# Optimization experiments

Measured on AMD Instinct MI355X. Metric: run time of the kernel, lower is better.

## Reference

```python
import jax, jax.numpy as jnp
import numpy as np
import math

N, E, D, H, C, ED = 50000, 400000, 128, 8, 16, 64
HC = H * C  # == D (required by residual)
EPS = 1e-5


def _gelu(x):
    return 0.5 * x * (1.0 + jax.lax.erf(x / math.sqrt(2.0)))


def _layer_norm(x, g, b):
    m = jnp.mean(x, axis=-1, keepdims=True)
    v = jnp.mean(jnp.square(x - m), axis=-1, keepdims=True)
    return (x - m) * jax.lax.rsqrt(v + EPS) * g + b


def _batch_norm(x, g, b):
    # BatchNorm1d training-mode math: stats over the batch (row) dim
    m = jnp.mean(x, axis=0)
    v = jnp.mean(jnp.square(x - m), axis=0)
    return (x - m) * jax.lax.rsqrt(v + EPS) * g + b


def setup_inputs() -> dict:
    key = jax.random.key(0)
    ks = jax.random.split(key, 40)
    s = 0.05
    inp = {
        "x": jax.random.normal(ks[0], (N, D), jnp.float32),
        "edge_index": jax.random.randint(ks[1], (2, E), 0, N, jnp.int64),
        "edge_attr": jax.random.normal(ks[2], (E, ED), jnp.float32),
        # attention projections
        "Wq": jax.random.normal(ks[3], (D, HC), jnp.float32) * s,
        "bq": jnp.zeros((HC,), jnp.float32),
        "Wk": jax.random.normal(ks[4], (D, HC), jnp.float32) * s,
        "bk": jnp.zeros((HC,), jnp.float32),
        "Wv": jax.random.normal(ks[5], (D, HC), jnp.float32) * s,
        "bv": jnp.zeros((HC,), jnp.float32),
        "We": jax.random.normal(ks[6], (ED, HC), jnp.float32) * s,  # no bias
        "Wke": jax.random.normal(ks[7], (3 * C, C), jnp.float32) * s,
        "bke": jnp.zeros((C,), jnp.float32),
        "Wve": jax.random.normal(ks[8], (3 * C, C), jnp.float32) * s,
        "bve": jnp.zeros((C,), jnp.float32),
        "Wfce": jax.random.normal(ks[9], (HC, ED), jnp.float32) * s,
        "bfce": jnp.zeros((ED,), jnp.float32),
        "lne_g": jnp.ones((ED,), jnp.float32),
        "lne_b": jnp.zeros((ED,), jnp.float32),
        "Wfcn": jax.random.normal(ks[10], (HC, D), jnp.float32) * s,
        "bfcn": jnp.zeros((D,), jnp.float32),
        "lnn_g": jnp.ones((D,), jnp.float32),
        "lnn_b": jnp.zeros((D,), jnp.float32),
        # FFN
        "W1n": jax.random.normal(ks[11], (D, 4 * D), jnp.float32) * s,
        "b1n": jnp.zeros((4 * D,), jnp.float32),
        "W2n": jax.random.normal(ks[12], (4 * D, D), jnp.float32) * s,
        "b2n": jnp.zeros((D,), jnp.float32),
        "W1e": jax.random.normal(ks[13], (ED, 4 * ED), jnp.float32) * s,
        "b1e": jnp.zeros((4 * ED,), jnp.float32),
        "W2e": jax.random.normal(ks[14], (4 * ED, ED), jnp.float32) * s,
        "b2e": jnp.zeros((ED,), jnp.float32),
        "bnn_g": jnp.ones((D,), jnp.float32),
        "bnn_b": jnp.zeros((D,), jnp.float32),
        "bne_g": jnp.ones((ED,), jnp.float32),
        "bne_b": jnp.zeros((ED,), jnp.float32),
    }
    return inp


def _forward(x, edge_attr, Wq, bq, Wk, bk, Wv, bv, We, Wke, bke, Wve, bve,
             Wfce, bfce, lne_g, lne_b, Wfcn, bfcn, lnn_g, lnn_b,
             W1n, b1n, W2n, b2n, W1e, b1e, W2e, b2e,
             bnn_g, bnn_b, bne_g, bne_b, edge_index):
    src = edge_index[0]  # j (source)
    dst = edge_index[1]  # i (target / aggregation index)

    Q = (x @ Wq + bq).reshape(N, H, C)
    K = (x @ Wk + bk).reshape(N, H, C)
    V = (x @ Wv + bv).reshape(N, H, C)

    Qi = Q[dst]                                  # [E,H,C]
    e = (edge_attr @ We).reshape(E, H, C)        # W_e(edge_attr)

    # K_e(cat([K_i, K_j, e])) as three C x C matmuls (avoids big concat)
    Wk1, Wk2, Wk3 = Wke[:C], Wke[C:2 * C], Wke[2 * C:]
    Knew = (jnp.einsum('ehc,cd->ehd', K[dst], Wk1)
            + jnp.einsum('ehc,cd->ehd', K[src], Wk2)
            + jnp.einsum('ehc,cd->ehd', e, Wk3) + bke)

    logits = jnp.sum(Qi * Knew, axis=-1) / math.sqrt(C)   # [E,H]
    # segment softmax over target nodes (PyG softmax)
    mx = jax.ops.segment_max(logits, dst, num_segments=N)  # [N,H]
    ex = jnp.exp(logits - mx[dst])
    den = jax.ops.segment_sum(ex, dst, num_segments=N)
    alpha = ex / (den[dst] + 1e-16)                        # [E,H]

    Wv1, Wv2, Wv3 = Wve[:C], Wve[C:2 * C], Wve[2 * C:]
    Vnew = (jnp.einsum('ehc,cd->ehd', V[dst], Wv1)
            + jnp.einsum('ehc,cd->ehd', V[src], Wv2)
            + jnp.einsum('ehc,cd->ehd', e, Wv3) + bve)

    edge_store = e * alpha[..., None]                      # saved self.edge_attr
    msg = Vnew * alpha[..., None]
    out = jax.ops.segment_sum(msg, dst, num_segments=N)    # [N,H,C]

    e_out = _layer_norm(edge_store.reshape(E, HC) @ Wfce + bfce, lne_g, lne_b) + edge_attr
    x_out = _layer_norm(out.reshape(N, HC) @ Wfcn + bfcn, lnn_g, lnn_b) + x

    # PoswiseFeedForwardNetwork
    x2 = _batch_norm(_gelu(x_out @ W1n + b1n) @ W2n + b2n, bnn_g, bnn_b) + x_out
    e2 = _batch_norm(_gelu(e_out @ W1e + b1e) @ W2e + b2e, bne_g, bne_b) + e_out
    return jax.nn.softplus(x2), jax.nn.softplus(e2)


def reference(x, edge_index, edge_attr, Wq, bq, Wk, bk, Wv, bv, We, Wke, bke,
              Wve, bve, Wfce, bfce, lne_g, lne_b, Wfcn, bfcn, lnn_g, lnn_b,
              W1n, b1n, W2n, b2n, W1e, b1e, W2e, b2e, bnn_g, bnn_b, bne_g, bne_b):
    return _forward(x, edge_attr, Wq, bq, Wk, bk, Wv, bv, We, Wke, bke, Wve, bve,
                    Wfce, bfce, lne_g, lne_b, Wfcn, bfcn, lnn_g, lnn_b,
                    W1n, b1n, W2n, b2n, W1e, b1e, W2e, b2e,
                    bnn_g, bnn_b, bne_g, bne_b, edge_index)
```

## Files before the change

### kernel.cpp

```cpp
#include <hip/hip_runtime.h>
#include <math.h>
#include <stdint.h>

#define N_NODES 50000
#define E_EDGES 400000
#define DIM 128
#define HEADS 8
#define CH 16
#define EDIM 64
#define HCDIM 128

#define EPCHUNK 100000
#define NODE_WAVES 4

using bf16x8 = __attribute__((ext_vector_type(8))) short;
using f32x4v = __attribute__((ext_vector_type(4))) float;


__global__ void fill_kernel(float* p, float v, int n) {
    int i = blockIdx.x * blockDim.x + threadIdx.x;
    if (i < n) p[i] = v;
}

__global__ void concat3_kernel(const float* __restrict__ a, const float* __restrict__ b,
                               const float* __restrict__ c, float* __restrict__ o) {
    int i = blockIdx.x * 256 + threadIdx.x;
    if (i < 128) o[i] = a[i];
    else if (i < 256) o[i] = b[i - 128];
    else if (i < 384) o[i] = c[i - 256];
}

__device__ inline float gelu_f(float x) {
    return 0.5f * x * (1.0f + erff(x * 0.70710678118654752f));
}

__device__ inline float softplus_f(float x) {
    return x > 20.f ? x : log1pf(expf(x));
}

__device__ inline unsigned short f32_to_bf16_rn(float f) {
    unsigned u = __float_as_uint(f);
    u += 0x7FFFu + ((u >> 16) & 1u);
    return (unsigned short)(u >> 16);
}
__device__ inline float bf16_to_f32(unsigned short h) {
    return __uint_as_float((unsigned)h << 16);
}

__global__ __launch_bounds__(256) void wsplit_kernel(
    const float* __restrict__ W, unsigned short* __restrict__ hi,
    unsigned short* __restrict__ lo, int K, int N)
{
    int idx = blockIdx.x * 256 + threadIdx.x;
    if (idx >= K * N) return;
    int n = idx / K, k = idx - n * K;
    float x = W[(size_t)k * N + n];
    unsigned short h = f32_to_bf16_rn(x);
    hi[idx] = h;
    lo[idx] = f32_to_bf16_rn(x - bf16_to_f32(h));
}

__global__ __launch_bounds__(256) void wsplit_perm_kernel(
    const float* __restrict__ W, unsigned short* __restrict__ hi,
    unsigned short* __restrict__ lo, int K, int N)
{
    int idx = blockIdx.x * 256 + threadIdx.x;
    if (idx >= K * N) return;
    int n = idx / K, k = idx - n * K;
    int s = k & 31, base = k & ~31;
    int lgp = s >> 3, j = s & 7;
    int ksrc = base + ((j < 4) ? (lgp * 4 + j) : (16 + lgp * 4 + (j - 4)));
    float x = W[(size_t)ksrc * N + n];
    unsigned short h = f32_to_bf16_rn(x);
    hi[idx] = h;
    lo[idx] = f32_to_bf16_rn(x - bf16_to_f32(h));
}

template<int BN>
__global__ __launch_bounds__(256) void gemm_mfma(
    const float* __restrict__ A,
    const unsigned short* __restrict__ Whi, const unsigned short* __restrict__ Wlo,
    const float* __restrict__ bias, const float* __restrict__ ascale,
    float* __restrict__ C, int M, int K, int Nc, int act, int cmode)
{
    constexpr int MT = (BN == 128) ? 4 : 2;
    __shared__ bf16x8 As[2][4][128];

    const int tid = threadIdx.x;
    const int w = tid >> 6, lane = tid & 63;
    const int l15 = lane & 15, lg = lane >> 4;
    const int m0 = blockIdx.y * 128;
    const int n0 = blockIdx.x * BN;
    const int rowbase = (BN == 128) ? (w >> 1) * 64 : w * 32;
    const int colbase = (BN == 128) ? (w & 1) * 64 : 0;
    const int k16 = K >> 4;

    f32x4v acc[MT][4];
#pragma unroll
    for (int i = 0; i < MT; ++i)
#pragma unroll
        for (int j = 0; j < 4; ++j)
#pragma unroll
            for (int cidx = 0; cidx < 4; ++cidx) acc[i][j][cidx] = 0.f;

    for (int k0 = 0; k0 < K; k0 += 32) {
#pragma unroll
        for (int it = 0; it < 2; ++it) {
            int row = w * 16 + l15 + it * 64;
            int ar = m0 + row;
            float v[8];
            if (ar < M) {
                const float* ap = A + (size_t)ar * K + k0 + lg * 8;
                *(float4*)&v[0] = *(const float4*)ap;
                *(float4*)&v[4] = *(const float4*)(ap + 4);
                if (ascale) {
                    float s = ascale[(size_t)ar * k16 + ((k0 >> 4) + (lg >> 1))];
#pragma unroll
                    for (int j = 0; j < 8; ++j) v[j] *= s;
                }
            } else {
#pragma unroll
                for (int j = 0; j < 8; ++j) v[j] = 0.f;
            }
            bf16x8 gh, gl;
#pragma unroll
            for (int j = 0; j < 8; ++j) {
                unsigned short h = f32_to_bf16_rn(v[j]);
                gh[j] = (short)h;
                gl[j] = (short)f32_to_bf16_rn(v[j] - bf16_to_f32(h));
            }
            As[0][lg][row] = gh;
            As[1][lg][row] = gl;
        }
        bf16x8 bh[4], bl[4];
#pragma unroll
        for (int nt = 0; nt < 4; ++nt) {
            size_t off = (size_t)(n0 + colbase + nt * 16 + l15) * K + k0 + lg * 8;
            bh[nt] = *(const bf16x8*)(Whi + off);
            bl[nt] = *(const bf16x8*)(Wlo + off);
        }
        __syncthreads();
#pragma unroll
        for (int mt = 0; mt < MT; ++mt) {
            int arow = rowbase + mt * 16 + l15;
            bf16x8 ah = As[0][lg][arow];
            bf16x8 al = As[1][lg][arow];
#pragma unroll
            for (int nt = 0; nt < 4; ++nt) {
                acc[mt][nt] = __builtin_amdgcn_mfma_f32_16x16x32_bf16(ah, bh[nt], acc[mt][nt], 0, 0, 0);
                acc[mt][nt] = __builtin_amdgcn_mfma_f32_16x16x32_bf16(al, bh[nt], acc[mt][nt], 0, 0, 0);
                acc[mt][nt] = __builtin_amdgcn_mfma_f32_16x16x32_bf16(ah, bl[nt], acc[mt][nt], 0, 0, 0);
            }
        }
        __syncthreads();
    }

#pragma unroll
    for (int nt = 0; nt < 4; ++nt) {
        int col = n0 + colbase + nt * 16 + l15;
        float bb = bias ? bias[col] : 0.f;
#pragma unroll
        for (int mt = 0; mt < MT; ++mt) {
#pragma unroll
            for (int i = 0; i < 4; ++i) {
                int r = m0 + rowbase + mt * 16 + lg * 4 + i;
                if (r < M) {
                    float o = acc[mt][nt][i] + bb;
                    if (act == 1) o = gelu_f(o);
                    if (cmode == 1) {
                        C[(size_t)(col >> 7) * ((size_t)N_NODES * HCDIM) + (size_t)r * HCDIM + (col & 127)] = o;
                    } else {
                        C[(size_t)r * Nc + col] = o;
                    }
                }
            }
        }
    }
}

static inline void launch_mfma(const float* A, const unsigned short* Whi, const unsigned short* Wlo,
                               const float* bias, const float* ascale, float* C,
                               int M, int K, int Nc, int act, int cmode, hipStream_t stream)
{
    int gy = (M + 127) / 128;
    if (Nc % 128 == 0)
        gemm_mfma<128><<<dim3(Nc / 128, gy), dim3(256), 0, stream>>>(A, Whi, Wlo, bias, ascale, C, M, K, Nc, act, cmode);
    else
        gemm_mfma<64><<<dim3(Nc / 64, gy), dim3(256), 0, stream>>>(A, Whi, Wlo, bias, ascale, C, M, K, Nc, act, cmode);
}

template<int MT, int K1, int NH, int N2, int ACT1, int ASC, int LN2>
__global__ __launch_bounds__(256) void ffn2_nobar(
    const float* __restrict__ A,
    const unsigned short* __restrict__ W1hi, const unsigned short* __restrict__ W1lo,
    const float* __restrict__ b1,
    const unsigned short* __restrict__ W2hi, const unsigned short* __restrict__ W2lo,
    const float* __restrict__ b2,
    const float* __restrict__ ascale,
    const float* __restrict__ lng, const float* __restrict__ lnb,
    const float* __restrict__ resid,
    float* __restrict__ Cout, int M)
{
    constexpr int NK = K1 / 32;
    constexpr int NT2 = N2 / 16;
    constexpr int NI = NH / 16;
    constexpr int NP = NH / 32;
    const int tid = threadIdx.x;
    const int w = tid >> 6, lane = tid & 63;
    const int l15 = lane & 15, lg = lane >> 4;
    const int row0 = (blockIdx.x * 4 + w) * (MT * 16);

    bf16x8 aAh[MT][NK], aAl[MT][NK];
#pragma unroll
    for (int mt = 0; mt < MT; ++mt) {
        int r = row0 + mt * 16 + l15;
#pragma unroll
        for (int ks = 0; ks < NK; ++ks) {
            float v[8];
            if (r < M) {
                const float* ap = A + (size_t)r * K1 + ks * 32 + lg * 8;
                *(float4*)&v[0] = *(const float4*)ap;
                *(float4*)&v[4] = *(const float4*)(ap + 4);
            } else {
#pragma unroll
                for (int j = 0; j < 8; ++j) v[j] = 0.f;
            }
            bf16x8 gh, gl;
#pragma unroll
            for (int j = 0; j < 8; ++j) {
                unsigned short h = f32_to_bf16_rn(v[j]);
                gh[j] = (short)h;
                gl[j] = (short)f32_to_bf16_rn(v[j] - bf16_to_f32(h));
            }
            aAh[mt][ks] = gh;
            aAl[mt][ks] = gl;
        }
    }

    f32x4v oacc[MT][NT2];
#pragma unroll
    for (int mt = 0; mt < MT; ++mt)
#pragma unroll
        for (int nt = 0; nt < NT2; ++nt)
#pragma unroll
            for (int c = 0; c < 4; ++c) oacc[mt][nt][c] = 0.f;

    for (int p = 0; p < NP; ++p) {
        bf16x8 hh[MT], hl[MT];
#pragma unroll
        for (int half = 0; half < 2; ++half) {
            const int it = p * 2 + half;
            f32x4v h[MT];
#pragma unroll
            for (int mt = 0; mt < MT; ++mt)
#pragma unroll
                for (int c = 0; c < 4; ++c) h[mt][c] = 0.f;
#pragma unroll
            for (int ks = 0; ks < NK; ++ks) {
                size_t off = (size_t)(it * 16 + l15) * K1 + ks * 32 + lg * 8;
                bf16x8 xh = *(const bf16x8*)(W1hi + off);
                bf16x8 xl = *(const bf16x8*)(W1lo + off);
#pragma unroll
                for (int mt = 0; mt < MT; ++mt) {
                    h[mt] = __builtin_amdgcn_mfma_f32_16x16x32_bf16(xh, aAh[mt][ks], h[mt], 0, 0, 0);
                    h[mt] = __builtin_amdgcn_mfma_f32_16x16x32_bf16(xl, aAh[mt][ks], h[mt], 0, 0, 0);
                    h[mt] = __builtin_amdgcn_mfma_f32_16x16x32_bf16(xh, aAl[mt][ks], h[mt], 0, 0, 0);
                }
            }
            float b1a[4] = {0.f, 0.f, 0.f, 0.f};
            if (b1) *(float4*)b1a = *(const float4*)(b1 + it * 16 + lg * 4);
#pragma unroll
            for (int mt = 0; mt < MT; ++mt) {
                float sc = 1.f;
                if (ASC) {
                    int r = row0 + mt * 16 + l15;
                    sc = (r < M) ? ascale[(size_t)r * NI + it] : 0.f;
                }
#pragma unroll
                for (int i = 0; i < 4; ++i) {
                    float o = h[mt][i] + b1a[i];
                    if (ACT1) o = gelu_f(o);
                    if (ASC) o *= sc;
                    unsigned short oh = f32_to_bf16_rn(o);
                    hh[mt][half * 4 + i] = (short)oh;
                    hl[mt][half * 4 + i] = (short)f32_to_bf16_rn(o - bf16_to_f32(oh));
                }
            }
        }
#pragma unroll
        for (int nt2 = 0; nt2 < NT2; ++nt2) {
            size_t off2 = (size_t)(nt2 * 16 + l15) * NH + p * 32 + lg * 8;
            bf16x8 x2h = *(const bf16x8*)(W2hi + off2);
            bf16x8 x2l = *(const bf16x8*)(W2lo + off2);
#pragma unroll
            for (int mt = 0; mt < MT; ++mt) {
                oacc[mt][nt2] = __builtin_amdgcn_mfma_f32_16x16x32_bf16(x2h, hh[mt], oacc[mt][nt2], 0, 0, 0);
                oacc[mt][nt2] = __builtin_amdgcn_mfma_f32_16x16x32_bf16(x2l, hh[mt], oacc[mt][nt2], 0, 0, 0);
                oacc[mt][nt2] = __builtin_amdgcn_mfma_f32_16x16x32_bf16(x2h, hl[mt], oacc[mt][nt2], 0, 0, 0);
            }
        }
    }

    float b2a[NT2][4];
#pragma unroll
    for (int nt2 = 0; nt2 < NT2; ++nt2) {
        if (b2) *(float4*)b2a[nt2] = *(const float4*)(b2 + nt2 * 16 + lg * 4);
        else { b2a[nt2][0] = 0.f; b2a[nt2][1] = 0.f; b2a[nt2][2] = 0.f; b2a[nt2][3] = 0.f; }
    }
    if (LN2) {
        float ga[NT2][4], bba[NT2][4];
#pragma unroll
        for (int nt2 = 0; nt2 < NT2; ++nt2) {
            *(float4*)ga[nt2] = *(const float4*)(lng + nt2 * 16 + lg * 4);
            *(float4*)bba[nt2] = *(const float4*)(lnb + nt2 * 16 + lg * 4);
        }
#pragma unroll
        for (int mt = 0; mt < MT; ++mt) {
            int r = row0 + mt * 16 + l15;
            float o[NT2][4];
            float s = 0.f;
#pragma unroll
            for (int nt2 = 0; nt2 < NT2; ++nt2)
#pragma unroll
                for (int i = 0; i < 4; ++i) { o[nt2][i] = oacc[mt][nt2][i] + b2a[nt2][i]; s += o[nt2][i]; }
            s += __shfl_xor(s, 16); s += __shfl_xor(s, 32);
            float mean = s * (1.f / (float)N2);
            float q = 0.f;
#pragma unroll
            for (int nt2 = 0; nt2 < NT2; ++nt2)
#pragma unroll
                for (int i = 0; i < 4; ++i) { o[nt2][i] -= mean; q += o[nt2][i] * o[nt2][i]; }
            q += __shfl_xor(q, 16); q += __shfl_xor(q, 32);
            float inv = rsqrtf(q * (1.f / (float)N2) + 1e-5f);
            if (r < M) {
#pragma unroll
                for (int nt2 = 0; nt2 < NT2; ++nt2) {
                    float4 rv = *(const float4*)(resid + (size_t)r * N2 + nt2 * 16 + lg * 4);
                    float4 ov;
                    ov.x = o[nt2][0] * inv * ga[nt2][0] + bba[nt2][0] + rv.x;
                    ov.y = o[nt2][1] * inv * ga[nt2][1] + bba[nt2][1] + rv.y;
                    ov.z = o[nt2][2] * inv * ga[nt2][2] + bba[nt2][2] + rv.z;
                    ov.w = o[nt2][3] * inv * ga[nt2][3] + bba[nt2][3] + rv.w;
                    *(float4*)(Cout + (size_t)r * N2 + nt2 * 16 + lg * 4) = ov;
                }
            }
        }
    } else {
#pragma unroll
        for (int mt = 0; mt < MT; ++mt) {
            int r = row0 + mt * 16 + l15;
            if (r < M) {
#pragma unroll
                for (int nt2 = 0; nt2 < NT2; ++nt2) {
                    float4 ov;
                    ov.x = oacc[mt][nt2][0] + b2a[nt2][0];
                    ov.y = oacc[mt][nt2][1] + b2a[nt2][1];
                    ov.z = oacc[mt][nt2][2] + b2a[nt2][2];
                    ov.w = oacc[mt][nt2][3] + b2a[nt2][3];
                    *(float4*)(Cout + (size_t)r * N2 + nt2 * 16 + lg * 4) = ov;
                }
            }
        }
    }
}

__global__ __launch_bounds__(256) void wex_kernel(
    const float* __restrict__ We, const float* __restrict__ X, float* __restrict__ out)
{
    int idx = blockIdx.x * 256 + threadIdx.x;
    if (idx >= 64 * 128) return;
    int k = idx >> 7, hj = idx & 127, h = hj >> 4, j = hj & 15;
    float s = 0.f;
#pragma unroll
    for (int c = 0; c < 16; ++c) s += We[k * 128 + h * 16 + c] * X[c * 16 + j];
    out[idx] = s;
}

__global__ __launch_bounds__(256) void qk_pre_kernel(
    const float* __restrict__ Q, const float* __restrict__ K,
    const float* __restrict__ Wke, const float* __restrict__ bke,
    float* __restrict__ A2, float* __restrict__ c0)
{
    __shared__ float wk1[256], wk2[256], bks[16];
    for (int i = threadIdx.x; i < 256; i += 256) { wk1[i] = Wke[i]; wk2[i] = Wke[256 + i]; }
    if (threadIdx.x < 16) bks[threadIdx.x] = bke[threadIdx.x];
    __syncthreads();
    int idx = blockIdx.x * 256 + threadIdx.x;
    int j = idx & 15; int dh = idx >> 4; int h = dh & 7; int d = dh >> 3;
    if (d >= N_NODES) return;
    const float* q = Q + (size_t)d * HCDIM + h * CH;
    const float* k = K + (size_t)d * HCDIM + h * CH;
    float qv[16], kv[16];
#pragma unroll
    for (int t = 0; t < 4; ++t) {
        *(float4*)&qv[t * 4] = *(const float4*)(q + t * 4);
        *(float4*)&kv[t * 4] = *(const float4*)(k + t * 4);
    }
    float a2 = 0.f;
#pragma unroll
    for (int t = 0; t < 16; ++t) a2 += wk2[j * 16 + t] * qv[t];
    A2[idx] = a2;
    float kn = bks[j];
#pragma unroll
    for (int c = 0; c < 16; ++c) kn += kv[c] * wk1[c * 16 + j];
    float t = qv[j] * kn;
    t += __shfl_xor(t, 1); t += __shfl_xor(t, 2); t += __shfl_xor(t, 4); t += __shfl_xor(t, 8);
    if (j == 0) c0[dh] = t;
}

__global__ __launch_bounds__(256) void logits_kernel(
    const float* __restrict__ Q, const float* __restrict__ K,
    const float* __restrict__ A2, const float* __restrict__ c0,
    const float* __restrict__ ep3,
    const int* __restrict__ src, const int* __restrict__ dst,
    float* __restrict__ logits, int e0, int ecnt)
{
    int idx = blockIdx.x * 256 + threadIdx.x;
    if (idx >= ecnt * HEADS) return;
    int el = idx >> 3, h = idx & 7, e = e0 + el;
    int s = src[e], d = dst[e];
    const float* q  = Q  + (size_t)d * HCDIM + h * CH;
    const float* a2 = A2 + (size_t)d * HCDIM + h * CH;
    const float* ks = K  + (size_t)s * HCDIM + h * CH;
    const float* ep = ep3 + (size_t)el * HCDIM + h * CH;
    float acc = c0[(size_t)d * HEADS + h];
    float qv[16], av[16], kv[16], ev[16];
#pragma unroll
    for (int t = 0; t < 4; ++t) {
        *(float4*)&qv[t * 4] = *(const float4*)(q + t * 4);
        *(float4*)&av[t * 4] = *(const float4*)(a2 + t * 4);
        *(float4*)&kv[t * 4] = *(const float4*)(ks + t * 4);
        *(float4*)&ev[t * 4] = *(const float4*)(ep + t * 4);
    }
#pragma unroll
    for (int t = 0; t < 16; ++t) acc += av[t] * kv[t] + qv[t] * ev[t];
    logits[(size_t)e * HEADS + h] = acc * 0.25f;
}

__global__ __launch_bounds__(256) void count_kernel(const int* __restrict__ dst, int* __restrict__ cnt) {
    int e = blockIdx.x * 256 + threadIdx.x;
    if (e < E_EDGES) atomicAdd(&cnt[dst[e]], 1);
}

__global__ __launch_bounds__(1024) void scan_kernel(
    const int* __restrict__ cnt, int* __restrict__ rowptr, int* __restrict__ cursor, int n)
{
    __shared__ int buf[1024];
    __shared__ int base;
    int tid = threadIdx.x;
    if (tid == 0) { base = 0; rowptr[0] = 0; }
    __syncthreads();
    for (int t0 = 0; t0 < n; t0 += 1024) {
        int i = t0 + tid;
        int v = (i < n) ? cnt[i] : 0;
        buf[tid] = v;
        __syncthreads();
        for (int off = 1; off < 1024; off <<= 1) {
            int add = (tid >= off) ? buf[tid - off] : 0;
            __syncthreads();
            buf[tid] += add;
            __syncthreads();
        }
        if (i < n) { rowptr[i + 1] = base + buf[tid]; cursor[i] = base + buf[tid] - v; }
        __syncthreads();
        if (tid == 0) base += buf[1023];
        __syncthreads();
    }
}

__global__ __launch_bounds__(256) void scatter_kernel(
    const int* __restrict__ dst, int* __restrict__ cursor, int* __restrict__ eidx) {
    int e = blockIdx.x * 256 + threadIdx.x;
    if (e < E_EDGES) {
        int p = atomicAdd(&cursor[dst[e]], 1);
        eidx[p] = e;
    }
}

__global__ __launch_bounds__(256) void node_attn_kernel(
    const float* __restrict__ Vb, const float* __restrict__ edge_attr,
    float* __restrict__ logits,
    const int* __restrict__ rowptr, const int* __restrict__ eidx,
    const int* __restrict__ src,
    const float* __restrict__ Wve, const float* __restrict__ bve,
    const float* __restrict__ WeWv3, float* __restrict__ aggout)
{
    __shared__ float wv1s[256], wv2s[256], bvs[16];
    __shared__ float stage[NODE_WAVES][640];

    for (int i = threadIdx.x; i < 256; i += 256) { wv1s[i] = Wve[i]; wv2s[i] = Wve[256 + i]; }
    if (threadIdx.x < 16) bvs[threadIdx.x] = bve[threadIdx.x];
    __syncthreads();

    int w = threadIdx.x >> 6, lane = threadIdx.x & 63;
    int d = blockIdx.x * NODE_WAVES + w;
    int r0 = rowptr[d], r1 = rowptr[d + 1], deg = r1 - r0;
    int h = lane >> 3, kg = lane & 7;

    if (deg == 0) {
        aggout[(size_t)d * HCDIM + lane] = 0.f;
        aggout[(size_t)d * HCDIM + 64 + lane] = 0.f;
    } else {
        float m[8], ssum[8];
#pragma unroll
        for (int t = 0; t < 8; ++t) { m[t] = -INFINITY; ssum[t] = 0.f; }
        for (int i = r0 + lane; i < r1; i += 64) {
            int e = eidx[i];
            const float* lp = logits + (size_t)e * HEADS;
            float l[8];
            *(float4*)&l[0] = *(const float4*)lp;
            *(float4*)&l[4] = *(const float4*)(lp + 4);
#pragma unroll
            for (int t = 0; t < 8; ++t) m[t] = fmaxf(m[t], l[t]);
        }
#pragma unroll
        for (int o = 1; o < 64; o <<= 1) {
#pragma unroll
            for (int t = 0; t < 8; ++t) m[t] = fmaxf(m[t], __shfl_xor(m[t], o));
        }
        for (int i = r0 + lane; i < r1; i += 64) {
            int e = eidx[i];
            const float* lp = logits + (size_t)e * HEADS;
            float l[8];
            *(float4*)&l[0] = *(const float4*)lp;
            *(float4*)&l[4] = *(const float4*)(lp + 4);
#pragma unroll
            for (int t = 0; t < 8; ++t) ssum[t] += expf(l[t] - m[t]);
        }
#pragma unroll
        for (int o = 1; o < 64; o <<= 1) {
#pragma unroll
            for (int t = 0; t < 8; ++t) ssum[t] += __shfl_xor(ssum[t], o);
        }
        float mh = m[0], dd = ssum[0];
#pragma unroll
        for (int t = 1; t < 8; ++t) { if (h == t) { mh = m[t]; dd = ssum[t]; } }
        float den = dd + 1e-16f;

        float wea[8] = {0.f, 0.f, 0.f, 0.f, 0.f, 0.f, 0.f, 0.f};
        float av0 = 0.f, av1 = 0.f;
        for (int i = r0; i < r1; ++i) {
            int e = eidx[i];
            float lg = logits[(size_t)e * HEADS + h];
            float alpha = expf(lg - mh) / den;
            if (kg == 0) logits[(size_t)e * HEADS + h] = alpha;
            int s = src[e];
            const float* ea = edge_attr + (size_t)e * EDIM + kg * 8;
            float ev[8];
            *(float4*)&ev[0] = *(const float4*)ea;
            *(float4*)&ev[4] = *(const float4*)(ea + 4);
#pragma unroll
            for (int t = 0; t < 8; ++t) wea[t] += alpha * ev[t];
            float2 vv = *(const float2*)(Vb + (size_t)s * HCDIM + h * CH + kg * 2);
            av0 += alpha * vv.x;
            av1 += alpha * vv.y;
        }
        float* st = stage[w];
#pragma unroll
        for (int t = 0; t < 8; ++t) st[h * 64 + kg * 8 + t] = wea[t];
        st[512 + h * 16 + kg * 2] = av0;
        st[512 + h * 16 + kg * 2 + 1] = av1;
    }
    __syncthreads();
    if (deg > 0) {
        float* st = stage[w];
        int c0i = kg * 2;
        float acc0 = bvs[c0i], acc1 = bvs[c0i + 1];
        const float* vd = Vb + (size_t)d * HCDIM + h * CH;
#pragma unroll
        for (int j = 0; j < 16; ++j) {
            float vj = vd[j];
            float a = st[512 + h * 16 + j];
            acc0 += vj * wv1s[j * 16 + c0i] + a * wv2s[j * 16 + c0i];
            acc1 += vj * wv1s[j * 16 + c0i + 1] + a * wv2s[j * 16 + c0i + 1];
        }
        const float* w3 = WeWv3 + h * 16 + c0i;
#pragma unroll 16
        for (int k = 0; k < 64; ++k) {
            float wv = st[h * 64 + k];
            float2 w2v = *(const float2*)(w3 + k * 128);
            acc0 += wv * w2v.x;
            acc1 += wv * w2v.y;
        }
        aggout[(size_t)d * HCDIM + h * CH + c0i] = acc0;
        aggout[(size_t)d * HCDIM + h * CH + c0i + 1] = acc1;
    }
}

__global__ __launch_bounds__(256) void ln_res_kernel(
    float* __restrict__ y, const float* __restrict__ g, const float* __restrict__ b,
    const float* __restrict__ res, int rows, int w)
{
    int wave = threadIdx.x >> 6;
    int lane = threadIdx.x & 63;
    int nw = blockDim.x >> 6;
    for (int r = blockIdx.x * nw + wave; r < rows; r += gridDim.x * nw) {
        size_t base = (size_t)r * w;
        float v0 = y[base + lane];
        float v1 = (w == 128) ? y[base + 64 + lane] : 0.f;
        float s = v0 + v1;
#pragma unroll
        for (int o = 32; o; o >>= 1) s += __shfl_xor(s, o);
        float m = s / (float)w;
        float d0 = v0 - m;
        float d1 = (w == 128) ? (v1 - m) : 0.f;
        float q = d0 * d0 + d1 * d1;
#pragma unroll
        for (int o = 32; o; o >>= 1) q += __shfl_xor(q, o);
        float inv = rsqrtf(q / (float)w + 1e-5f);
        y[base + lane] = d0 * inv * g[lane] + b[lane] + res[base + lane];
        if (w == 128)
            y[base + 64 + lane] = d1 * inv * g[64 + lane] + b[64 + lane] + res[base + 64 + lane];
    }
}

__global__ __launch_bounds__(256) void bn_stats_kernel(
    const float* __restrict__ y, float* __restrict__ colsum, float* __restrict__ colsq,
    int rows, int cols)
{
    __shared__ float ss[256], sq[256];
    int tid = threadIdx.x;
    int col = tid % cols;
    int rsub = tid / cols;
    int rstep = blockDim.x / cols;
    float ls = 0.f, lq = 0.f;
    for (int r = blockIdx.x * rstep + rsub; r < rows; r += gridDim.x * rstep) {
        float v = y[(size_t)r * cols + col];
        ls += v;
        lq += v * v;
    }
    ss[tid] = ls;
    sq[tid] = lq;
    __syncthreads();
    if (tid < cols) {
        for (int o = cols; o < 256; o += cols) { ls += ss[tid + o]; lq += sq[tid + o]; }
        atomicAdd(&colsum[tid], ls);
        atomicAdd(&colsq[tid], lq);
    }
}

__global__ __launch_bounds__(256) void bn_apply_softplus_kernel(
    const float* __restrict__ y, const float* __restrict__ res,
    const float* __restrict__ colsum, const float* __restrict__ colsq,
    const float* __restrict__ g, const float* __restrict__ b,
    float* __restrict__ out, int rows, int cols)
{
    int idx = blockIdx.x * blockDim.x + threadIdx.x;
    int n = rows * cols;
    if (idx >= n) return;
    int c = idx % cols;
    float m = colsum[c] / (float)rows;
    float var = colsq[c] / (float)rows - m * m;
    float inv = rsqrtf(var + 1e-5f);
    float v = (y[idx] - m) * inv * g[c] + b[c] + res[idx];
    out[idx] = softplus_f(v);
}


extern "C" void kernel_launch(void* const* d_in, const int* in_sizes, int n_in,
                              void* d_out, int out_size, void* d_ws, size_t ws_size,
                              hipStream_t stream) {
    const float* x         = (const float*)d_in[0];
    const int*   ei        = (const int*)d_in[1];
    const float* edge_attr = (const float*)d_in[2];
    const float* Wq  = (const float*)d_in[3];
    const float* bq  = (const float*)d_in[4];
    const float* Wk  = (const float*)d_in[5];
    const float* bk  = (const float*)d_in[6];
    const float* Wv  = (const float*)d_in[7];
    const float* bv  = (const float*)d_in[8];
    const float* We  = (const float*)d_in[9];
    const float* Wke = (const float*)d_in[10];
    const float* bke = (const float*)d_in[11];
    const float* Wve = (const float*)d_in[12];
    const float* bve = (const float*)d_in[13];
    const float* Wfce = (const float*)d_in[14];
    const float* bfce = (const float*)d_in[15];
    const float* lne_g = (const float*)d_in[16];
    const float* lne_b = (const float*)d_in[17];
    const float* Wfcn = (const float*)d_in[18];
    const float* bfcn = (const float*)d_in[19];
    const float* lnn_g = (const float*)d_in[20];
    const float* lnn_b = (const float*)d_in[21];
    const float* W1n = (const float*)d_in[22];
    const float* b1n = (const float*)d_in[23];
    const float* W2n = (const float*)d_in[24];
    const float* b2n = (const float*)d_in[25];
    const float* W1e = (const float*)d_in[26];
    const float* b1e = (const float*)d_in[27];
    const float* W2e = (const float*)d_in[28];
    const float* b2e = (const float*)d_in[29];
    const float* bnn_g = (const float*)d_in[30];
    const float* bnn_b = (const float*)d_in[31];
    const float* bne_g = (const float*)d_in[32];
    const float* bne_b = (const float*)d_in[33];

    const int* src = ei;
    const int* dst = ei + E_EDGES;

    float* ws = (float*)d_ws;
    const size_t M64   = (size_t)E_EDGES * EDIM;
    const size_t NODE2 = (size_t)N_NODES * HCDIM;

    float* regionR = ws;
    float* Qb  = regionR;
    float* Kb  = regionR + NODE2;
    float* Vb  = regionR + 2 * NODE2;

    float* overlayY = ws + M64;
    float* logits = overlayY;
    float* c0buf  = logits + (size_t)E_EDGES * HEADS;
    int*   cnt_i    = (int*)(c0buf + (size_t)N_NODES * HEADS);
    int*   rowptr_i = cnt_i + N_NODES;
    int*   cursor_i = rowptr_i + N_NODES + 1;
    int*   eidx_i   = cursor_i + N_NODES;
    float* aggout = (float*)(((uintptr_t)(eidx_i + E_EDGES) + 15) & ~(uintptr_t)15);
    float* y_n    = aggout + NODE2;
    float* x_out  = y_n + NODE2;
    float* y_e    = overlayY;
    float* epbig  = y_n;

    float* e_out = ws + 2 * M64;
    float* A2buf = e_out;

    float* tail = ws + 3 * M64;
    float* colsum_n = tail;
    float* colsq_n  = tail + 128;
    float* colsum_e = tail + 256;
    float* colsq_e  = tail + 320;
    float* WeK3  = tail + 384;
    float* WeWv3 = WeK3 + 8192;
    float* bqkv  = WeWv3 + 8192;

    unsigned short* wsp = (unsigned short*)(bqkv + 384);
    unsigned short* QKV_s  = wsp;
    unsigned short* WeK3_s = QKV_s  + 2 * 49152;
    unsigned short* We_s   = WeK3_s + 2 * 8192;
    unsigned short* Wfce_s = We_s   + 2 * 8192;
    unsigned short* Wfcn_s = Wfce_s + 2 * 8192;
    unsigned short* W1n_s  = Wfcn_s + 2 * 16384;
    unsigned short* W2n_s  = W1n_s  + 2 * 65536;
    unsigned short* W1e_s  = W2n_s  + 2 * 65536;
    unsigned short* W2e_s  = W1e_s  + 2 * 16384;

    dim3 blk(256);

    fill_kernel<<<dim3(2), blk, 0, stream>>>(colsum_n, 0.f, 384);
    fill_kernel<<<dim3((N_NODES + 255) / 256), blk, 0, stream>>>((float*)cnt_i, 0.f, N_NODES);

    wex_kernel<<<dim3(32), blk, 0, stream>>>(We, Wke + 2 * CH * CH, WeK3);
    wex_kernel<<<dim3(32), blk, 0, stream>>>(We, Wve + 2 * CH * CH, WeWv3);

    wsplit_kernel<<<dim3(64), blk, 0, stream>>>(Wq, QKV_s,          QKV_s + 49152,          128, 128);
    wsplit_kernel<<<dim3(64), blk, 0, stream>>>(Wk, QKV_s + 16384,  QKV_s + 49152 + 16384,  128, 128);
    wsplit_kernel<<<dim3(64), blk, 0, stream>>>(Wv, QKV_s + 32768,  QKV_s + 49152 + 32768,  128, 128);
    wsplit_kernel<<<dim3(32), blk, 0, stream>>>(WeK3, WeK3_s, WeK3_s + 8192,  64, 128);
    wsplit_kernel<<<dim3(32), blk, 0, stream>>>(We,   We_s,   We_s + 8192,    64, 128);
    wsplit_perm_kernel<<<dim3(32), blk, 0, stream>>>(Wfce, Wfce_s, Wfce_s + 8192,  128, 64);
    wsplit_kernel<<<dim3(64), blk, 0, stream>>>(Wfcn, Wfcn_s, Wfcn_s + 16384, 128, 128);
    wsplit_kernel<<<dim3(256), blk, 0, stream>>>(W1n, W1n_s, W1n_s + 65536,   128, 512);
    wsplit_perm_kernel<<<dim3(256), blk, 0, stream>>>(W2n, W2n_s, W2n_s + 65536,   512, 128);
    wsplit_kernel<<<dim3(64), blk, 0, stream>>>(W1e, W1e_s, W1e_s + 16384,    64, 256);
    wsplit_perm_kernel<<<dim3(64), blk, 0, stream>>>(W2e, W2e_s, W2e_s + 16384,    256, 64);
    concat3_kernel<<<dim3(2), blk, 0, stream>>>(bq, bk, bv, bqkv);

    launch_mfma(x, QKV_s, QKV_s + 49152, bqkv, nullptr, Qb, N_NODES, 128, 384, 0, 1, stream);

    qk_pre_kernel<<<dim3(N_NODES * HCDIM / 256), blk, 0, stream>>>(Qb, Kb, Wke, bke, A2buf, c0buf);

    count_kernel<<<dim3((E_EDGES + 255) / 256), blk, 0, stream>>>(dst, cnt_i);
    scan_kernel<<<dim3(1), dim3(1024), 0, stream>>>(cnt_i, rowptr_i, cursor_i, N_NODES);
    scatter_kernel<<<dim3((E_EDGES + 255) / 256), blk, 0, stream>>>(dst, cursor_i, eidx_i);

    for (int e0 = 0; e0 < E_EDGES; e0 += EPCHUNK) {
        launch_mfma(edge_attr + (size_t)e0 * EDIM, WeK3_s, WeK3_s + 8192, nullptr, nullptr,
                    epbig, EPCHUNK, EDIM, HCDIM, 0, 0, stream);
        logits_kernel<<<dim3((EPCHUNK * HEADS + 255) / 256), blk, 0, stream>>>(
            Qb, Kb, A2buf, c0buf, epbig, src, dst, logits, e0, EPCHUNK);
    }

    node_attn_kernel<<<dim3(N_NODES / NODE_WAVES), blk, 0, stream>>>(
        Vb, edge_attr, logits, rowptr_i, eidx_i, src, Wve, bve, WeWv3, aggout);

    ffn2_nobar<2, 64, 128, 64, 0, 1, 1><<<dim3(E_EDGES / 128), blk, 0, stream>>>(
        edge_attr, We_s, We_s + 8192, nullptr, Wfce_s, Wfce_s + 8192, bfce,
        logits, lne_g, lne_b, edge_attr, e_out, E_EDGES);

    launch_mfma(aggout, Wfcn_s, Wfcn_s + 16384, bfcn, nullptr, x_out, N_NODES, HCDIM, DIM, 0, 0, stream);
    ln_res_kernel<<<dim3(12500), blk, 0, stream>>>(x_out, lnn_g, lnn_b, x, N_NODES, DIM);

    ffn2_nobar<1, 128, 512, 128, 1, 0, 0><<<dim3((N_NODES + 63) / 64), blk, 0, stream>>>(
        x_out, W1n_s, W1n_s + 65536, b1n, W2n_s, W2n_s + 65536, b2n,
        nullptr, nullptr, nullptr, nullptr, y_n, N_NODES);
    bn_stats_kernel<<<dim3(256), blk, 0, stream>>>(y_n, colsum_n, colsq_n, N_NODES, DIM);
    {
        int n = N_NODES * DIM;
        bn_apply_softplus_kernel<<<dim3((n + 255) / 256), blk, 0, stream>>>(
            y_n, x_out, colsum_n, colsq_n, bnn_g, bnn_b, (float*)d_out, N_NODES, DIM);
    }

    ffn2_nobar<2, 64, 256, 64, 1, 0, 0><<<dim3(E_EDGES / 128), blk, 0, stream>>>(
        e_out, W1e_s, W1e_s + 16384, b1e, W2e_s, W2e_s + 16384, b2e,
        nullptr, nullptr, nullptr, nullptr, y_e, E_EDGES);
    bn_stats_kernel<<<dim3(256), blk, 0, stream>>>(y_e, colsum_e, colsq_e, E_EDGES, EDIM);
    {
        int n = E_EDGES * EDIM;
        bn_apply_softplus_kernel<<<dim3((n + 255) / 256), blk, 0, stream>>>(
            y_e, e_out, colsum_e, colsq_e, bne_g, bne_b, (float*)d_out + (size_t)N_NODES * DIM, E_EDGES, EDIM);
    }
}
```

Measured before the change: 2.043 ms.

## Fuse edge projection GEMM with logits computation and streamline softmax

Replaces the chunked edge-projection GEMM plus separate logits kernel with a single MFMA kernel that computes the per-edge projection in registers and reduces it directly into attention logits. This avoids writing and re-reading a 400000x128 float intermediate and drops eight launches. It also adds a single-pass softmax path for nodes with at most 64 incoming edges and pads the shared staging buffer to reduce LDS bank conflicts. In exchange, the fused epilogue does uncoalesced scalar gathers of Q/A2/K rows per lane and uses shuffle reductions.

```diff
diff --git a/kernel.cpp b/kernel.cpp
--- a/kernel.cpp
+++ b/kernel.cpp
@@ -10,7 +10,6 @@
 #define EDIM 64
 #define HCDIM 128
 
-#define EPCHUNK 100000
 #define NODE_WAVES 4
 
 using bf16x8 = __attribute__((ext_vector_type(8))) short;
@@ -189,6 +188,102 @@
         gemm_mfma<64><<<dim3(Nc / 64, gy), dim3(256), 0, stream>>>(A, Whi, Wlo, bias, ascale, C, M, K, Nc, act, cmode);
 }
 
+__global__ __launch_bounds__(256) void eproj_logits_kernel(
+    const float* __restrict__ EA,
+    const unsigned short* __restrict__ Whi, const unsigned short* __restrict__ Wlo,
+    const float* __restrict__ Qp, const float* __restrict__ Kp,
+    const float* __restrict__ A2, const float* __restrict__ c0,
+    const int* __restrict__ src, const int* __restrict__ dst,
+    float* __restrict__ logits)
+{
+    __shared__ bf16x8 As[2][4][128];
+    const int tid = threadIdx.x;
+    const int w = tid >> 6, lane = tid & 63;
+    const int l15 = lane & 15, lg = lane >> 4;
+    const int m0 = blockIdx.x * 128;
+    const int rowbase = (w >> 1) * 64;
+    const int colbase = (w & 1) * 64;
+
+    f32x4v acc[4][4];
+#pragma unroll
+    for (int i = 0; i < 4; ++i)
+#pragma unroll
+        for (int j = 0; j < 4; ++j)
+#pragma unroll
+            for (int cidx = 0; cidx < 4; ++cidx) acc[i][j][cidx] = 0.f;
+
+    for (int k0 = 0; k0 < EDIM; k0 += 32) {
+#pragma unroll
+        for (int it = 0; it < 2; ++it) {
+            int row = w * 16 + l15 + it * 64;
+            const float* ap = EA + (size_t)(m0 + row) * EDIM + k0 + lg * 8;
+            float v[8];
+            *(float4*)&v[0] = *(const float4*)ap;
+            *(float4*)&v[4] = *(const float4*)(ap + 4);
+            bf16x8 gh, gl;
+#pragma unroll
+            for (int j = 0; j < 8; ++j) {
+                unsigned short h = f32_to_bf16_rn(v[j]);
+                gh[j] = (short)h;
+                gl[j] = (short)f32_to_bf16_rn(v[j] - bf16_to_f32(h));
+            }
+            As[0][lg][row] = gh;
+            As[1][lg][row] = gl;
+        }
+        bf16x8 bh[4], bl[4];
+#pragma unroll
+        for (int nt = 0; nt < 4; ++nt) {
+            size_t off = (size_t)(colbase + nt * 16 + l15) * EDIM + k0 + lg * 8;
+            bh[nt] = *(const bf16x8*)(Whi + off);
+            bl[nt] = *(const bf16x8*)(Wlo + off);
+        }
+        __syncthreads();
+#pragma unroll
+        for (int mt = 0; mt < 4; ++mt) {
+            int arow = rowbase + mt * 16 + l15;
+            bf16x8 ah = As[0][lg][arow];
+            bf16x8 al = As[1][lg][arow];
+#pragma unroll
+            for (int nt = 0; nt < 4; ++nt) {
+                acc[mt][nt] = __builtin_amdgcn_mfma_f32_16x16x32_bf16(ah, bh[nt], acc[mt][nt], 0, 0, 0);
+                acc[mt][nt] = __builtin_amdgcn_mfma_f32_16x16x32_bf16(al, bh[nt], acc[mt][nt], 0, 0, 0);
+                acc[mt][nt] = __builtin_amdgcn_mfma_f32_16x16x32_bf16(ah, bl[nt], acc[mt][nt], 0, 0, 0);
+            }
+        }
+        __syncthreads();
+    }
+
+    const int hbase = (w & 1) * 4;
+#pragma unroll
+    for (int mt = 0; mt < 4; ++mt) {
+#pragma unroll
+        for (int i = 0; i < 4; ++i) {
+            int e = m0 + rowbase + mt * 16 + lg * 4 + i;
+            int d = dst[e], s = src[e];
+            const float* qd  = Qp + (size_t)d * HCDIM + hbase * 16;
+            const float* a2d = A2 + (size_t)d * HCDIM + hbase * 16;
+            const float* ks  = Kp + (size_t)s * HCDIM + hbase * 16;
+            float part[4];
+#pragma unroll
+            for (int nt = 0; nt < 4; ++nt) {
+                int cc = nt * 16 + l15;
+                part[nt] = acc[mt][nt][i] * qd[cc] + a2d[cc] * ks[cc];
+            }
+#pragma unroll
+            for (int o = 1; o < 16; o <<= 1) {
+#pragma unroll
+                for (int nt = 0; nt < 4; ++nt) part[nt] += __shfl_xor(part[nt], o);
+            }
+            if (l15 == 0) {
+                const float* c0d = c0 + (size_t)d * HEADS + hbase;
+#pragma unroll
+                for (int nt = 0; nt < 4; ++nt)
+                    logits[(size_t)e * HEADS + hbase + nt] = (c0d[nt] + part[nt]) * 0.25f;
+            }
+        }
+    }
+}
+
 template<int MT, int K1, int NH, int N2, int ACT1, int ASC, int LN2>
 __global__ __launch_bounds__(256) void ffn2_nobar(
     const float* __restrict__ A,
@@ -406,35 +501,6 @@
     float t = qv[j] * kn;
     t += __shfl_xor(t, 1); t += __shfl_xor(t, 2); t += __shfl_xor(t, 4); t += __shfl_xor(t, 8);
     if (j == 0) c0[dh] = t;
-}
-
-__global__ __launch_bounds__(256) void logits_kernel(
-    const float* __restrict__ Q, const float* __restrict__ K,
-    const float* __restrict__ A2, const float* __restrict__ c0,
-    const float* __restrict__ ep3,
-    const int* __restrict__ src, const int* __restrict__ dst,
-    float* __restrict__ logits, int e0, int ecnt)
-{
-    int idx = blockIdx.x * 256 + threadIdx.x;
-    if (idx >= ecnt * HEADS) return;
-    int el = idx >> 3, h = idx & 7, e = e0 + el;
-    int s = src[e], d = dst[e];
-    const float* q  = Q  + (size_t)d * HCDIM + h * CH;
-    const float* a2 = A2 + (size_t)d * HCDIM + h * CH;
-    const float* ks = K  + (size_t)s * HCDIM + h * CH;
-    const float* ep = ep3 + (size_t)el * HCDIM + h * CH;
-    float acc = c0[(size_t)d * HEADS + h];
-    float qv[16], av[16], kv[16], ev[16];
-#pragma unroll
-    for (int t = 0; t < 4; ++t) {
-        *(float4*)&qv[t * 4] = *(const float4*)(q + t * 4);
-        *(float4*)&av[t * 4] = *(const float4*)(a2 + t * 4);
-        *(float4*)&kv[t * 4] = *(const float4*)(ks + t * 4);
-        *(float4*)&ev[t * 4] = *(const float4*)(ep + t * 4);
-    }
-#pragma unroll
-    for (int t = 0; t < 16; ++t) acc += av[t] * kv[t] + qv[t] * ev[t];
-    logits[(size_t)e * HEADS + h] = acc * 0.25f;
 }
 
 __global__ __launch_bounds__(256) void count_kernel(const int* __restrict__ dst, int* __restrict__ cnt) {
@@ -486,7 +552,7 @@
     const float* __restrict__ WeWv3, float* __restrict__ aggout)
 {
     __shared__ float wv1s[256], wv2s[256], bvs[16];
-    __shared__ float stage[NODE_WAVES][640];
+    __shared__ float stage[NODE_WAVES][656];
 
     for (int i = threadIdx.x; i < 256; i += 256) { wv1s[i] = Wve[i]; wv2s[i] = Wve[256 + i]; }
     if (threadIdx.x < 16) bvs[threadIdx.x] = bve[threadIdx.x];
@@ -502,35 +568,62 @@
         aggout[(size_t)d * HCDIM + 64 + lane] = 0.f;
     } else {
         float m[8], ssum[8];
-#pragma unroll
-        for (int t = 0; t < 8; ++t) { m[t] = -INFINITY; ssum[t] = 0.f; }
-        for (int i = r0 + lane; i < r1; i += 64) {
-            int e = eidx[i];
-            const float* lp = logits + (size_t)e * HEADS;
+        if (deg <= 64) {
             float l[8];
-            *(float4*)&l[0] = *(const float4*)lp;
-            *(float4*)&l[4] = *(const float4*)(lp + 4);
-#pragma unroll
-            for (int t = 0; t < 8; ++t) m[t] = fmaxf(m[t], l[t]);
-        }
-#pragma unroll
-        for (int o = 1; o < 64; o <<= 1) {
-#pragma unroll
-            for (int t = 0; t < 8; ++t) m[t] = fmaxf(m[t], __shfl_xor(m[t], o));
-        }
-        for (int i = r0 + lane; i < r1; i += 64) {
-            int e = eidx[i];
-            const float* lp = logits + (size_t)e * HEADS;
-            float l[8];
-            *(float4*)&l[0] = *(const float4*)lp;
-            *(float4*)&l[4] = *(const float4*)(lp + 4);
-#pragma unroll
-            for (int t = 0; t < 8; ++t) ssum[t] += expf(l[t] - m[t]);
-        }
-#pragma unroll
-        for (int o = 1; o < 64; o <<= 1) {
-#pragma unroll
-            for (int t = 0; t < 8; ++t) ssum[t] += __shfl_xor(ssum[t], o);
+            if (r0 + lane < r1) {
+                int e = eidx[r0 + lane];
+                const float* lp = logits + (size_t)e * HEADS;
+                *(float4*)&l[0] = *(const float4*)lp;
+                *(float4*)&l[4] = *(const float4*)(lp + 4);
+            } else {
+#pragma unroll
+                for (int t = 0; t < 8; ++t) l[t] = -INFINITY;
+            }
+#pragma unroll
+            for (int t = 0; t < 8; ++t) m[t] = l[t];
+#pragma unroll
+            for (int o = 1; o < 64; o <<= 1) {
+#pragma unroll
+                for (int t = 0; t < 8; ++t) m[t] = fmaxf(m[t], __shfl_xor(m[t], o));
+            }
+#pragma unroll
+            for (int t = 0; t < 8; ++t) ssum[t] = expf(l[t] - m[t]);
+#pragma unroll
+            for (int o = 1; o < 64; o <<= 1) {
+#pragma unroll
+                for (int t = 0; t < 8; ++t) ssum[t] += __shfl_xor(ssum[t], o);
+            }
+        } else {
+#pragma unroll
+            for (int t = 0; t < 8; ++t) { m[t] = -INFINITY; ssum[t] = 0.f; }
+            for (int i = r0 + lane; i < r1; i += 64) {
+                int e = eidx[i];
+                const float* lp = logits + (size_t)e * HEADS;
+                float l[8];
+                *(float4*)&l[0] = *(const float4*)lp;
+                *(float4*)&l[4] = *(const float4*)(lp + 4);
+#pragma unroll
+                for (int t = 0; t < 8; ++t) m[t] = fmaxf(m[t], l[t]);
+            }
+#pragma unroll
+            for (int o = 1; o < 64; o <<= 1) {
+#pragma unroll
+                for (int t = 0; t < 8; ++t) m[t] = fmaxf(m[t], __shfl_xor(m[t], o));
+            }
+            for (int i = r0 + lane; i < r1; i += 64) {
+                int e = eidx[i];
+                const float* lp = logits + (size_t)e * HEADS;
+                float l[8];
+                *(float4*)&l[0] = *(const float4*)lp;
+                *(float4*)&l[4] = *(const float4*)(lp + 4);
+#pragma unroll
+                for (int t = 0; t < 8; ++t) ssum[t] += expf(l[t] - m[t]);
+            }
+#pragma unroll
+            for (int o = 1; o < 64; o <<= 1) {
+#pragma unroll
+                for (int t = 0; t < 8; ++t) ssum[t] += __shfl_xor(ssum[t], o);
+            }
         }
         float mh = m[0], dd = ssum[0];
 #pragma unroll
@@ -557,9 +650,9 @@
         }
         float* st = stage[w];
 #pragma unroll
-        for (int t = 0; t < 8; ++t) st[h * 64 + kg * 8 + t] = wea[t];
-        st[512 + h * 16 + kg * 2] = av0;
-        st[512 + h * 16 + kg * 2 + 1] = av1;
+        for (int t = 0; t < 8; ++t) st[h * 65 + kg * 8 + t] = wea[t];
+        st[520 + h * 17 + kg * 2] = av0;
+        st[520 + h * 17 + kg * 2 + 1] = av1;
     }
     __syncthreads();
     if (deg > 0) {
@@ -570,14 +663,14 @@
 #pragma unroll
         for (int j = 0; j < 16; ++j) {
             float vj = vd[j];
-            float a = st[512 + h * 16 + j];
+            float a = st[520 + h * 17 + j];
             acc0 += vj * wv1s[j * 16 + c0i] + a * wv2s[j * 16 + c0i];
             acc1 += vj * wv1s[j * 16 + c0i + 1] + a * wv2s[j * 16 + c0i + 1];
         }
         const float* w3 = WeWv3 + h * 16 + c0i;
 #pragma unroll 16
         for (int k = 0; k < 64; ++k) {
-            float wv = st[h * 64 + k];
+            float wv = st[h * 65 + k];
             float2 w2v = *(const float2*)(w3 + k * 128);
             acc0 += wv * w2v.x;
             acc1 += wv * w2v.y;
@@ -718,7 +811,6 @@
     float* y_n    = aggout + NODE2;
     float* x_out  = y_n + NODE2;
     float* y_e    = overlayY;
-    float* epbig  = y_n;
 
     float* e_out = ws + 2 * M64;
     float* A2buf = e_out;
@@ -772,12 +864,8 @@
     scan_kernel<<<dim3(1), dim3(1024), 0, stream>>>(cnt_i, rowptr_i, cursor_i, N_NODES);
     scatter_kernel<<<dim3((E_EDGES + 255) / 256), blk, 0, stream>>>(dst, cursor_i, eidx_i);
 
-    for (int e0 = 0; e0 < E_EDGES; e0 += EPCHUNK) {
-        launch_mfma(edge_attr + (size_t)e0 * EDIM, WeK3_s, WeK3_s + 8192, nullptr, nullptr,
-                    epbig, EPCHUNK, EDIM, HCDIM, 0, 0, stream);
-        logits_kernel<<<dim3((EPCHUNK * HEADS + 255) / 256), blk, 0, stream>>>(
-            Qb, Kb, A2buf, c0buf, epbig, src, dst, logits, e0, EPCHUNK);
-    }
+    eproj_logits_kernel<<<dim3(E_EDGES / 128), blk, 0, stream>>>(
+        edge_attr, WeK3_s, WeK3_s + 8192, Qb, Kb, A2buf, c0buf, src, dst, logits);
 
     node_attn_kernel<<<dim3(N_NODES / NODE_WAVES), blk, 0, stream>>>(
         Vb, edge_attr, logits, rowptr_i, eidx_i, src, Wve, bve, WeWv3, aggout);
```

Measured after the change: 1.810 ms. -11.4%, faster.
